# Kernel optimization log

Measured on AMD Instinct MI355X. Metric: run time of the kernel, lower is better.

The kernel has to match this reference:

```python
import jax, jax.numpy as jnp
import numpy as np

N, E, G = 20000, 400000, 200
IN, HID, OUT, H = 8, 64, 32, 4
EPS = 1e-5
NEG_SLOPE = 0.2


def _gatv2(x, src, dst, Wl, bl, Wr, br, att, bias, n, heads, c):
    # lin_l (source messages) and lin_r (target queries)
    xl = (x @ Wl + bl).reshape(n, heads, c)
    xr = (x @ Wr + br).reshape(n, heads, c)
    # per-edge GATv2 score: att . LeakyReLU(x_l[j] + x_r[i])
    e = jax.nn.leaky_relu(xl[src] + xr[dst], NEG_SLOPE)          # [E,H,C]
    score = jnp.einsum('ehc,hc->eh', e, att)                     # [E,H]
    # softmax over incoming edges of each target node
    m = jax.ops.segment_max(score, dst, num_segments=n)
    ex = jnp.exp(score - m[dst])
    den = jax.ops.segment_sum(ex, dst, num_segments=n)
    alpha = ex / den[dst]                                        # [E,H]
    out = jax.ops.segment_sum(alpha[:, :, None] * xl[src], dst, num_segments=n)
    return out.mean(axis=1) + bias                               # concat=False: head mean


def _layernorm(x, g, b):
    mu = x.mean(-1, keepdims=True)
    var = ((x - mu) ** 2).mean(-1, keepdims=True)
    return (x - mu) * jax.lax.rsqrt(var + EPS) * g + b


def setup_inputs() -> dict:
    key = jax.random.key(0)
    ks = jax.random.split(key, 16)
    s = 0.1
    inp = {
        'x': jax.random.normal(ks[0], (N, IN), jnp.float32),
        'edge_index': jax.random.randint(ks[1], (2, E), 0, N, jnp.int64 if jax.config.jax_enable_x64 else jnp.int32),
        'batch': jnp.sort(jax.random.randint(ks[2], (N,), 0, G)),
        'Wl1': jax.random.normal(ks[3], (IN, H * HID), jnp.float32) * s,
        'bl1': jnp.zeros((H * HID,), jnp.float32),
        'Wr1': jax.random.normal(ks[4], (IN, H * HID), jnp.float32) * s,
        'br1': jnp.zeros((H * HID,), jnp.float32),
        'att1': jax.random.normal(ks[5], (H, HID), jnp.float32) * s,
        'b1': jnp.zeros((HID,), jnp.float32),
        'ln1_g': jnp.ones((HID,), jnp.float32),
        'ln1_b': jnp.zeros((HID,), jnp.float32),
        'Wl2': jax.random.normal(ks[6], (HID, H * OUT), jnp.float32) * s,
        'bl2': jnp.zeros((H * OUT,), jnp.float32),
        'Wr2': jax.random.normal(ks[7], (HID, H * OUT), jnp.float32) * s,
        'br2': jnp.zeros((H * OUT,), jnp.float32),
        'att2': jax.random.normal(ks[8], (H, OUT), jnp.float32) * s,
        'b2': jnp.zeros((OUT,), jnp.float32),
        'ln2_g': jnp.ones((OUT,), jnp.float32),
        'ln2_b': jnp.zeros((OUT,), jnp.float32),
    }
    return inp


def reference(x, edge_index, batch, Wl1, bl1, Wr1, br1, att1, b1, ln1_g, ln1_b,
              Wl2, bl2, Wr2, br2, att2, b2, ln2_g, ln2_b):
    n = x.shape[0]
    loop = jnp.arange(n, dtype=edge_index.dtype)  # add_self_loops=True (PyG default)
    src = jnp.concatenate([edge_index[0], loop])
    dst = jnp.concatenate([edge_index[1], loop])

    h = _gatv2(x, src, dst, Wl1, bl1, Wr1, br1, att1, b1, n, H, HID)
    h = jax.nn.relu(_layernorm(h, ln1_g, ln1_b))
    h = _gatv2(h, src, dst, Wl2, bl2, Wr2, br2, att2, b2, n, H, OUT)
    h = jax.nn.relu(_layernorm(h, ln2_g, ln2_b))

    # global mean pool per graph
    cnt = jax.ops.segment_sum(jnp.ones((n,), h.dtype), batch, num_segments=G)
    pooled = jax.ops.segment_sum(h, batch, num_segments=G)
    return pooled / jnp.maximum(cnt, 1.0)[:, None]
```

## Files before the change

kernel.cpp:

```cpp
#include <hip/hip_runtime.h>
#include <math.h>
#include <stdint.h>

#define NEG_SLOPE 0.2f
#define LN_EPS 1e-5f

typedef __attribute__((ext_vector_type(8))) short short8;
typedef __attribute__((ext_vector_type(4))) float f32x4;

__device__ __forceinline__ uint32_t pack_bf2(float a, float b) {
  uint32_t ua = __float_as_uint(a);
  uint32_t ub = __float_as_uint(b);
  ua = (ua + 0x7fffu + ((ua >> 16) & 1u)) >> 16;
  ub = (ub + 0x7fffu + ((ub >> 16) & 1u)) & 0xffff0000u;
  return ua | ub;
}
__device__ __forceinline__ float2 unpack_bf2(uint32_t u) {
  return make_float2(__uint_as_float(u << 16), __uint_as_float(u & 0xffff0000u));
}
__device__ __forceinline__ uint16_t bf16_rne(float f) {
  uint32_t u = __float_as_uint(f);
  return (uint16_t)((u + 0x7fffu + ((u >> 16) & 1u)) >> 16);
}

__global__ void hist_kernel(const int* __restrict__ ei, int E, int N, int* __restrict__ cnt) {
  int e = blockIdx.x * blockDim.x + threadIdx.x;
  if (e >= E + N) return;
  int dst = (e < E) ? ei[E + e] : (e - E);
  atomicAdd(&cnt[dst], 1);
}

__global__ __launch_bounds__(1024) void scan_kernel(const int* __restrict__ cnt,
                                                    int* __restrict__ offs,
                                                    int* __restrict__ cursor, int n) {
  __shared__ int wsum[16];
  int tid = threadIdx.x;
  int lane = tid & 63, w = tid >> 6;
  int PER = (n + 1023) >> 10;
  int base = tid * PER;
  int s = 0;
  for (int j = 0; j < PER; ++j) {
    int idx = base + j;
    s += (idx < n) ? cnt[idx] : 0;
  }
  int inc = s;
#pragma unroll
  for (int d = 1; d < 64; d <<= 1) {
    int t = __shfl_up(inc, d, 64);
    if (lane >= d) inc += t;
  }
  if (lane == 63) wsum[w] = inc;
  __syncthreads();
  int wpre = 0;
  for (int j = 0; j < w; ++j) wpre += wsum[j];
  int run = wpre + inc - s;
  for (int j = 0; j < PER; ++j) {
    int idx = base + j;
    if (idx < n) {
      offs[idx] = run;
      cursor[idx] = run;
      run += cnt[idx];
    }
  }
  if (tid == 1023) offs[n] = run;
}

__global__ void scatter_kernel(const int* __restrict__ ei, int E, int N,
                               int* __restrict__ cursor, int* __restrict__ esrc) {
  int e = blockIdx.x * blockDim.x + threadIdx.x;
  if (e >= E + N) return;
  int src, dst;
  if (e < E) { src = ei[e]; dst = ei[E + e]; }
  else       { src = e - E; dst = src; }
  int pos = atomicAdd(&cursor[dst], 1);
  esrc[pos] = src;
}

__global__ void prep_wt_kernel(const float* __restrict__ Wl, const float* __restrict__ Wr,
                               uint16_t* __restrict__ Wtb) {
  int idx = blockIdx.x * blockDim.x + threadIdx.x;
  if (idx >= 256 * 64) return;
  int c = idx >> 6, k = idx & 63;
  float v = (c < 128) ? Wl[k * 128 + c] : Wr[k * 128 + (c - 128)];
  Wtb[idx] = bf16_rne(v);
}

__global__ __launch_bounds__(256) void gemm1_kernel(
    const float* __restrict__ x,
    const float* __restrict__ Wl, const float* __restrict__ bl,
    const float* __restrict__ Wr, const float* __restrict__ br,
    uint32_t* __restrict__ xl1b, float* __restrict__ xr1, int N) {
  int tid = threadIdx.x;
  int c2 = tid & 127;
  int which = tid >> 7;
  float wl0[8], wl1[8], wr0[8], wr1[8];
#pragma unroll
  for (int k = 0; k < 8; ++k) {
    wl0[k] = Wl[k * 256 + 2 * c2]; wl1[k] = Wl[k * 256 + 2 * c2 + 1];
    wr0[k] = Wr[k * 256 + 2 * c2]; wr1[k] = Wr[k * 256 + 2 * c2 + 1];
  }
  float bl0 = bl[2 * c2], bl1v = bl[2 * c2 + 1];
  float br0 = br[2 * c2], br1v = br[2 * c2 + 1];
  int npair = (N + 1) >> 1;
  for (int pr = blockIdx.x; pr < npair; pr += gridDim.x) {
    int n = pr * 2 + which;
    if (n >= N) continue;
    float4 xa = ((const float4*)x)[n * 2];
    float4 xb = ((const float4*)x)[n * 2 + 1];
    float xs[8] = {xa.x, xa.y, xa.z, xa.w, xb.x, xb.y, xb.z, xb.w};
    float al0 = bl0, al1 = bl1v, ar0 = br0, ar1 = br1v;
#pragma unroll
    for (int k = 0; k < 8; ++k) {
      al0 = fmaf(xs[k], wl0[k], al0); al1 = fmaf(xs[k], wl1[k], al1);
      ar0 = fmaf(xs[k], wr0[k], ar0); ar1 = fmaf(xs[k], wr1[k], ar1);
    }
    xl1b[(size_t)n * 128 + c2] = pack_bf2(al0, al1);
    ((float2*)xr1)[(size_t)n * 128 + c2] = make_float2(ar0, ar1);
  }
}

__global__ __launch_bounds__(256) void gemm2_mfma_kernel(
    const uint16_t* __restrict__ h1b,
    const uint16_t* __restrict__ Wtb,
    const float* __restrict__ bl, const float* __restrict__ br,
    uint32_t* __restrict__ xl2b, float* __restrict__ xr2, int N) {
  int lane = threadIdx.x & 63;
  int w = threadIdx.x >> 6;
  int c0 = w << 6;
  int l15 = lane & 15, l4 = lane >> 4;
  int node = (blockIdx.x << 4) + l15;
  int nodec = node < N ? node : N - 1;
  const short8* hrow = (const short8*)(h1b + (size_t)nodec * 64);
  short8 b0 = hrow[l4];
  short8 b1 = hrow[4 + l4];
  f32x4 acc[4] = {{0.f,0.f,0.f,0.f},{0.f,0.f,0.f,0.f},{0.f,0.f,0.f,0.f},{0.f,0.f,0.f,0.f}};
#pragma unroll
  for (int t = 0; t < 4; ++t) {
    int row = c0 + (t << 4) + l15;
    const short8* wrow = (const short8*)(Wtb + (size_t)row * 64);
    short8 a0 = wrow[l4];
    short8 a1 = wrow[4 + l4];
    acc[t] = __builtin_amdgcn_mfma_f32_16x16x32_bf16(a0, b0, acc[t], 0, 0, 0);
    acc[t] = __builtin_amdgcn_mfma_f32_16x16x32_bf16(a1, b1, acc[t], 0, 0, 0);
  }
  if (node >= N) return;
  if (c0 < 128) {
#pragma unroll
    for (int t = 0; t < 4; ++t) {
      int q0 = c0 + (t << 4) + (l4 << 2);
      float4 bb = *(const float4*)(bl + q0);
      uint2 pk;
      pk.x = pack_bf2(acc[t][0] + bb.x, acc[t][1] + bb.y);
      pk.y = pack_bf2(acc[t][2] + bb.z, acc[t][3] + bb.w);
      *(uint2*)(xl2b + (size_t)node * 64 + (q0 >> 1)) = pk;
    }
  } else {
#pragma unroll
    for (int t = 0; t < 4; ++t) {
      int q0 = (c0 - 128) + (t << 4) + (l4 << 2);
      float4 bb = *(const float4*)(br + q0);
      float4 v = make_float4(acc[t][0] + bb.x, acc[t][1] + bb.y,
                             acc[t][2] + bb.z, acc[t][3] + bb.w);
      *(float4*)(xr2 + (size_t)node * 128 + q0) = v;
    }
  }
}

__global__ __launch_bounds__(256) void attn1_kernel(
    const uint32_t* __restrict__ xl1b, const float* __restrict__ xr1,
    const float* __restrict__ att, const float* __restrict__ b1,
    const float* __restrict__ g, const float* __restrict__ be,
    const int* __restrict__ offs, const int* __restrict__ esrc,
    uint32_t* __restrict__ h1b, int N) {
  int lane = threadIdx.x & 63;
  int i = blockIdx.x * (blockDim.x >> 6) + (threadIdx.x >> 6);
  if (i >= N) return;
  int cq = lane & 15;
  const uint2* xlb = (const uint2*)xl1b;
  float4 attq = ((const float4*)att)[lane];
  float4 attn_ = make_float4(NEG_SLOPE * attq.x, NEG_SLOPE * attq.y,
                             NEG_SLOPE * attq.z, NEG_SLOPE * attq.w);
  float4 xrq = ((const float4*)xr1)[(size_t)i * 64 + lane];
  float dA = 0.f, aA0 = 0.f, aA1 = 0.f, aA2 = 0.f, aA3 = 0.f;
  float dB = 0.f, aB0 = 0.f, aB1 = 0.f, aB2 = 0.f, aB3 = 0.f;
  int beg = offs[i], end = offs[i + 1];
  int p = beg;

#define EDGE1(U, DD, A0, A1, A2, A3)                                           \
  {                                                                            \
    float2 e0 = unpack_bf2(U.x), e1 = unpack_bf2(U.y);                         \
    float t0 = e0.x + xrq.x, t1 = e0.y + xrq.y;                                \
    float t2 = e1.x + xrq.z, t3 = e1.y + xrq.w;                                \
    float sc = t0 * (t0 > 0.f ? attq.x : attn_.x);                             \
    sc = fmaf(t1, (t1 > 0.f ? attq.y : attn_.y), sc);                          \
    sc = fmaf(t2, (t2 > 0.f ? attq.z : attn_.z), sc);                          \
    sc = fmaf(t3, (t3 > 0.f ? attq.w : attn_.w), sc);                          \
    sc += __shfl_xor(sc, 8, 64); sc += __shfl_xor(sc, 4, 64);                  \
    sc += __shfl_xor(sc, 2, 64); sc += __shfl_xor(sc, 1, 64);                  \
    float wgt = __expf(sc);                                                    \
    DD += wgt;                                                                 \
    A0 = fmaf(wgt, e0.x, A0); A1 = fmaf(wgt, e0.y, A1);                        \
    A2 = fmaf(wgt, e1.x, A2); A3 = fmaf(wgt, e1.y, A3);                        \
  }

  for (; p + 3 < end; p += 4) {
    int s0 = esrc[p], s1 = esrc[p + 1], s2 = esrc[p + 2], s3 = esrc[p + 3];
    uint2 u0 = xlb[(size_t)s0 * 64 + lane];
    uint2 u1 = xlb[(size_t)s1 * 64 + lane];
    uint2 u2 = xlb[(size_t)s2 * 64 + lane];
    uint2 u3 = xlb[(size_t)s3 * 64 + lane];
    EDGE1(u0, dA, aA0, aA1, aA2, aA3)
    EDGE1(u1, dB, aB0, aB1, aB2, aB3)
    EDGE1(u2, dA, aA0, aA1, aA2, aA3)
    EDGE1(u3, dB, aB0, aB1, aB2, aB3)
  }
  for (; p < end; ++p) {
    int s0 = esrc[p];
    uint2 u0 = xlb[(size_t)s0 * 64 + lane];
    EDGE1(u0, dA, aA0, aA1, aA2, aA3)
  }
#undef EDGE1

  float inv = 1.0f / (dA + dB);
  float v0 = (aA0 + aB0) * inv;
  float v1 = (aA1 + aB1) * inv;
  float v2 = (aA2 + aB2) * inv;
  float v3 = (aA3 + aB3) * inv;
  v0 += __shfl_xor(v0, 16, 64); v0 += __shfl_xor(v0, 32, 64);
  v1 += __shfl_xor(v1, 16, 64); v1 += __shfl_xor(v1, 32, 64);
  v2 += __shfl_xor(v2, 16, 64); v2 += __shfl_xor(v2, 32, 64);
  v3 += __shfl_xor(v3, 16, 64); v3 += __shfl_xor(v3, 32, 64);
  float4 b1q = ((const float4*)b1)[cq];
  v0 = 0.25f * v0 + b1q.x;
  v1 = 0.25f * v1 + b1q.y;
  v2 = 0.25f * v2 + b1q.z;
  v3 = 0.25f * v3 + b1q.w;
  float s1 = v0 + v1 + v2 + v3;
#pragma unroll
  for (int msk = 8; msk >= 1; msk >>= 1) s1 += __shfl_xor(s1, msk, 64);
  float mu = s1 * (1.0f / 64.0f);
  float d0 = v0 - mu, d1 = v1 - mu, d2 = v2 - mu, d3 = v3 - mu;
  float s2 = d0 * d0 + d1 * d1 + d2 * d2 + d3 * d3;
#pragma unroll
  for (int msk = 8; msk >= 1; msk >>= 1) s2 += __shfl_xor(s2, msk, 64);
  float rstd = rsqrtf(s2 * (1.0f / 64.0f) + LN_EPS);
  float4 gq = ((const float4*)g)[cq];
  float4 beq = ((const float4*)be)[cq];
  float y0 = fmaxf(fmaf(d0 * rstd, gq.x, beq.x), 0.f);
  float y1 = fmaxf(fmaf(d1 * rstd, gq.y, beq.y), 0.f);
  float y2 = fmaxf(fmaf(d2 * rstd, gq.z, beq.z), 0.f);
  float y3 = fmaxf(fmaf(d3 * rstd, gq.w, beq.w), 0.f);
  if (lane < 16) {
    uint2 pk;
    pk.x = pack_bf2(y0, y1);
    pk.y = pack_bf2(y2, y3);
    *(uint2*)(h1b + (size_t)i * 32 + cq * 2) = pk;
  }
}

__global__ __launch_bounds__(256) void attn2_kernel(
    const uint32_t* __restrict__ xl2b, const float* __restrict__ xr2,
    const float* __restrict__ att, const float* __restrict__ b2,
    const float* __restrict__ g, const float* __restrict__ be,
    const int* __restrict__ offs, const int* __restrict__ esrc,
    float* __restrict__ h2, int N) {
  int lane = threadIdx.x & 63;
  int i = blockIdx.x * (blockDim.x >> 6) + (threadIdx.x >> 6);
  if (i >= N) return;
  int cq = lane & 15;
  float2 attq = ((const float2*)att)[lane];
  float2 attn_ = make_float2(NEG_SLOPE * attq.x, NEG_SLOPE * attq.y);
  float2 xrq = ((const float2*)xr2)[(size_t)i * 64 + lane];
  float dA = 0.f, aA0 = 0.f, aA1 = 0.f;
  float dB = 0.f, aB0 = 0.f, aB1 = 0.f;
  int beg = offs[i], end = offs[i + 1];
  int p = beg;

#define EDGE2(U, DD, A0, A1)                                                   \
  {                                                                            \
    float2 e0 = unpack_bf2(U);                                                 \
    float t0 = e0.x + xrq.x, t1 = e0.y + xrq.y;                                \
    float sc = t0 * (t0 > 0.f ? attq.x : attn_.x);                             \
    sc = fmaf(t1, (t1 > 0.f ? attq.y : attn_.y), sc);                          \
    sc += __shfl_xor(sc, 8, 64); sc += __shfl_xor(sc, 4, 64);                  \
    sc += __shfl_xor(sc, 2, 64); sc += __shfl_xor(sc, 1, 64);                  \
    float wgt = __expf(sc);                                                    \
    DD += wgt;                                                                 \
    A0 = fmaf(wgt, e0.x, A0); A1 = fmaf(wgt, e0.y, A1);                        \
  }

  for (; p + 3 < end; p += 4) {
    int s0 = esrc[p], s1 = esrc[p + 1], s2 = esrc[p + 2], s3 = esrc[p + 3];
    uint32_t u0 = xl2b[(size_t)s0 * 64 + lane];
    uint32_t u1 = xl2b[(size_t)s1 * 64 + lane];
    uint32_t u2 = xl2b[(size_t)s2 * 64 + lane];
    uint32_t u3 = xl2b[(size_t)s3 * 64 + lane];
    EDGE2(u0, dA, aA0, aA1)
    EDGE2(u1, dB, aB0, aB1)
    EDGE2(u2, dA, aA0, aA1)
    EDGE2(u3, dB, aB0, aB1)
  }
  for (; p < end; ++p) {
    int s0 = esrc[p];
    uint32_t u0 = xl2b[(size_t)s0 * 64 + lane];
    EDGE2(u0, dA, aA0, aA1)
  }
#undef EDGE2

  float inv = 1.0f / (dA + dB);
  float v0 = (aA0 + aB0) * inv;
  float v1 = (aA1 + aB1) * inv;
  v0 += __shfl_xor(v0, 16, 64); v0 += __shfl_xor(v0, 32, 64);
  v1 += __shfl_xor(v1, 16, 64); v1 += __shfl_xor(v1, 32, 64);
  float2 b2q = ((const float2*)b2)[cq];
  v0 = 0.25f * v0 + b2q.x;
  v1 = 0.25f * v1 + b2q.y;
  float s1 = v0 + v1;
#pragma unroll
  for (int msk = 8; msk >= 1; msk >>= 1) s1 += __shfl_xor(s1, msk, 64);
  float mu = s1 * (1.0f / 32.0f);
  float d0 = v0 - mu, d1 = v1 - mu;
  float s2 = d0 * d0 + d1 * d1;
#pragma unroll
  for (int msk = 8; msk >= 1; msk >>= 1) s2 += __shfl_xor(s2, msk, 64);
  float rstd = rsqrtf(s2 * (1.0f / 32.0f) + LN_EPS);
  float2 gq = ((const float2*)g)[cq];
  float2 beq = ((const float2*)be)[cq];
  float y0 = fmaxf(fmaf(d0 * rstd, gq.x, beq.x), 0.f);
  float y1 = fmaxf(fmaf(d1 * rstd, gq.y, beq.y), 0.f);
  if (lane < 16) ((float2*)h2)[(size_t)i * 16 + cq] = make_float2(y0, y1);
}

__global__ __launch_bounds__(256) void pool_kernel(const float* __restrict__ h2,
                                                   const int* __restrict__ batch,
                                                   float* __restrict__ out, int N) {
  int gidx = blockIdx.x;
  int a = 0, b = N;
  while (a < b) { int m = (a + b) >> 1; if (batch[m] < gidx) a = m + 1; else b = m; }
  int lo = a;
  b = N;
  while (a < b) { int m = (a + b) >> 1; if (batch[m] < gidx + 1) a = m + 1; else b = m; }
  int hi = a;
  int c = threadIdx.x & 31, r = threadIdx.x >> 5;
  float s = 0.f;
  for (int n = lo + r; n < hi; n += 8) s += h2[(size_t)n * 32 + c];
  __shared__ float buf[256];
  buf[threadIdx.x] = s;
  __syncthreads();
  if (threadIdx.x < 128) buf[threadIdx.x] += buf[threadIdx.x + 128];
  __syncthreads();
  if (threadIdx.x < 64) buf[threadIdx.x] += buf[threadIdx.x + 64];
  __syncthreads();
  if (threadIdx.x < 32) {
    float v = buf[threadIdx.x] + buf[threadIdx.x + 32];
    int cnt = hi - lo;
    out[gidx * 32 + threadIdx.x] = v / (float)(cnt > 0 ? cnt : 1);
  }
}

extern "C" void kernel_launch(void* const* d_in, const int* in_sizes, int n_in,
                              void* d_out, int out_size, void* d_ws, size_t ws_size,
                              hipStream_t stream) {
  const float* x    = (const float*)d_in[0];
  const int*   ei   = (const int*)d_in[1];
  const int*   batch= (const int*)d_in[2];
  const float* Wl1  = (const float*)d_in[3];
  const float* bl1  = (const float*)d_in[4];
  const float* Wr1  = (const float*)d_in[5];
  const float* br1  = (const float*)d_in[6];
  const float* att1 = (const float*)d_in[7];
  const float* b1   = (const float*)d_in[8];
  const float* ln1g = (const float*)d_in[9];
  const float* ln1b = (const float*)d_in[10];
  const float* Wl2  = (const float*)d_in[11];
  const float* bl2  = (const float*)d_in[12];
  const float* Wr2  = (const float*)d_in[13];
  const float* br2  = (const float*)d_in[14];
  const float* att2 = (const float*)d_in[15];
  const float* b2   = (const float*)d_in[16];
  const float* ln2g = (const float*)d_in[17];
  const float* ln2b = (const float*)d_in[18];

  int N = in_sizes[0] / 8;
  int E = in_sizes[1] / 2;
  int G = out_size / 32;

  char* ws = (char*)d_ws;
  size_t off = 0;
  auto alloc = [&](size_t bytes) -> void* {
    void* p = (void*)(ws + off);
    off += (bytes + 255) & ~(size_t)255;
    return p;
  };
  int*      cnt    = (int*)alloc((size_t)N * 4);
  int*      offs   = (int*)alloc((size_t)(N + 1) * 4);
  int*      cursor = (int*)alloc((size_t)N * 4);
  int*      esrc   = (int*)alloc((size_t)(E + N) * 4);
  uint32_t* xl1b   = (uint32_t*)alloc((size_t)N * 128 * 4);
  float*    xr1    = (float*)alloc((size_t)N * 256 * 4);
  uint32_t* h1b    = (uint32_t*)alloc((size_t)N * 64 * 2);
  uint16_t* Wtb    = (uint16_t*)alloc((size_t)256 * 64 * 2);
  uint32_t* xl2b   = (uint32_t*)alloc((size_t)N * 64 * 4);
  float*    xr2    = (float*)alloc((size_t)N * 128 * 4);
  float*    h2     = (float*)alloc((size_t)N * 32 * 4);

  hipMemsetAsync(cnt, 0, (size_t)N * 4, stream);

  int tot = E + N;
  hist_kernel<<<(tot + 255) / 256, 256, 0, stream>>>(ei, E, N, cnt);
  scan_kernel<<<1, 1024, 0, stream>>>(cnt, offs, cursor, N);
  scatter_kernel<<<(tot + 255) / 256, 256, 0, stream>>>(ei, E, N, cursor, esrc);
  prep_wt_kernel<<<64, 256, 0, stream>>>(Wl2, Wr2, Wtb);

  gemm1_kernel<<<2048, 256, 0, stream>>>(x, Wl1, bl1, Wr1, br1, xl1b, xr1, N);
  attn1_kernel<<<(N + 3) / 4, 256, 0, stream>>>(xl1b, xr1, att1, b1, ln1g, ln1b,
                                                offs, esrc, h1b, N);
  gemm2_mfma_kernel<<<(N + 15) / 16, 256, 0, stream>>>((const uint16_t*)h1b, Wtb, bl2, br2,
                                                       xl2b, xr2, N);
  attn2_kernel<<<(N + 3) / 4, 256, 0, stream>>>(xl2b, xr2, att2, b2, ln2g, ln2b,
                                                offs, esrc, h2, N);

  pool_kernel<<<G, 256, 0, stream>>>(h2, batch, (float*)d_out, N);
}
```

Baseline: 187.8 us.

## Fuse histogram into gemm1, weight prep into scatter, use DPP row reductions

Merges the destination histogram into the layer-1 linear kernel and the bf16 weight transpose into the CSR scatter kernel, removing two kernel launches. Replaces the xor-shuffle reductions over 16 lanes with DPP row operations, which avoid LDS-based permutes. Switches gather addressing to 32-bit index arithmetic to cut 64-bit multiply work. The fused kernels lengthen serial work inside gemm1 and the scatter, and the 32-bit index math relies on the buffer offsets fitting in 32 bits.

```diff
diff --git a/kernel.cpp b/kernel.cpp
--- a/kernel.cpp
+++ b/kernel.cpp
@@ -23,11 +23,52 @@
   return (uint16_t)((u + 0x7fffu + ((u >> 16) & 1u)) >> 16);
 }
 
-__global__ void hist_kernel(const int* __restrict__ ei, int E, int N, int* __restrict__ cnt) {
-  int e = blockIdx.x * blockDim.x + threadIdx.x;
-  if (e >= E + N) return;
-  int dst = (e < E) ? ei[E + e] : (e - E);
-  atomicAdd(&cnt[dst], 1);
+__device__ __forceinline__ float row16_sum(float x) {
+  x += __int_as_float(__builtin_amdgcn_mov_dpp(__float_as_int(x), 0xB1, 0xF, 0xF, true));
+  x += __int_as_float(__builtin_amdgcn_mov_dpp(__float_as_int(x), 0x4E, 0xF, 0xF, true));
+  x += __int_as_float(__builtin_amdgcn_mov_dpp(__float_as_int(x), 0x124, 0xF, 0xF, true));
+  x += __int_as_float(__builtin_amdgcn_mov_dpp(__float_as_int(x), 0x128, 0xF, 0xF, true));
+  return x;
+}
+
+__global__ __launch_bounds__(256) void gemm1_hist_kernel(
+    const float* __restrict__ x,
+    const float* __restrict__ Wl, const float* __restrict__ bl,
+    const float* __restrict__ Wr, const float* __restrict__ br,
+    uint32_t* __restrict__ xl1b, float* __restrict__ xr1, int N,
+    const int* __restrict__ ei, int E, int* __restrict__ cnt) {
+  int tid = threadIdx.x;
+  int c2 = tid & 127;
+  int which = tid >> 7;
+  float wl0[8], wl1[8], wr0[8], wr1[8];
+#pragma unroll
+  for (int k = 0; k < 8; ++k) {
+    wl0[k] = Wl[k * 256 + 2 * c2]; wl1[k] = Wl[k * 256 + 2 * c2 + 1];
+    wr0[k] = Wr[k * 256 + 2 * c2]; wr1[k] = Wr[k * 256 + 2 * c2 + 1];
+  }
+  float bl0 = bl[2 * c2], bl1v = bl[2 * c2 + 1];
+  float br0 = br[2 * c2], br1v = br[2 * c2 + 1];
+  int npair = (N + 1) >> 1;
+  for (int pr = blockIdx.x; pr < npair; pr += gridDim.x) {
+    int n = pr * 2 + which;
+    if (n >= N) continue;
+    float4 xa = ((const float4*)x)[n * 2];
+    float4 xb = ((const float4*)x)[n * 2 + 1];
+    float xs[8] = {xa.x, xa.y, xa.z, xa.w, xb.x, xb.y, xb.z, xb.w};
+    float al0 = bl0, al1 = bl1v, ar0 = br0, ar1 = br1v;
+#pragma unroll
+    for (int k = 0; k < 8; ++k) {
+      al0 = fmaf(xs[k], wl0[k], al0); al1 = fmaf(xs[k], wl1[k], al1);
+      ar0 = fmaf(xs[k], wr0[k], ar0); ar1 = fmaf(xs[k], wr1[k], ar1);
+    }
+    xl1b[(size_t)n * 128 + c2] = pack_bf2(al0, al1);
+    ((float2*)xr1)[(size_t)n * 128 + c2] = make_float2(ar0, ar1);
+  }
+  int tot = E + N;
+  for (int e = blockIdx.x * blockDim.x + tid; e < tot; e += gridDim.x * blockDim.x) {
+    int dst = (e < E) ? ei[E + e] : (e - E);
+    atomicAdd(&cnt[dst], 1);
+  }
 }
 
 __global__ __launch_bounds__(1024) void scan_kernel(const int* __restrict__ cnt,
@@ -66,7 +107,15 @@
 }
 
 __global__ void scatter_kernel(const int* __restrict__ ei, int E, int N,
-                               int* __restrict__ cursor, int* __restrict__ esrc) {
+                               int* __restrict__ cursor, int* __restrict__ esrc,
+                               const float* __restrict__ Wl2, const float* __restrict__ Wr2,
+                               uint16_t* __restrict__ Wtb) {
+  if (blockIdx.x < 64) {
+    int idx = blockIdx.x * 256 + threadIdx.x;
+    int c = idx >> 6, k = idx & 63;
+    float v = (c < 128) ? Wl2[k * 128 + c] : Wr2[k * 128 + (c - 128)];
+    Wtb[idx] = bf16_rne(v);
+  }
   int e = blockIdx.x * blockDim.x + threadIdx.x;
   if (e >= E + N) return;
   int src, dst;
@@ -74,49 +123,6 @@
   else       { src = e - E; dst = src; }
   int pos = atomicAdd(&cursor[dst], 1);
   esrc[pos] = src;
-}
-
-__global__ void prep_wt_kernel(const float* __restrict__ Wl, const float* __restrict__ Wr,
-                               uint16_t* __restrict__ Wtb) {
-  int idx = blockIdx.x * blockDim.x + threadIdx.x;
-  if (idx >= 256 * 64) return;
-  int c = idx >> 6, k = idx & 63;
-  float v = (c < 128) ? Wl[k * 128 + c] : Wr[k * 128 + (c - 128)];
-  Wtb[idx] = bf16_rne(v);
-}
-
-__global__ __launch_bounds__(256) void gemm1_kernel(
-    const float* __restrict__ x,
-    const float* __restrict__ Wl, const float* __restrict__ bl,
-    const float* __restrict__ Wr, const float* __restrict__ br,
-    uint32_t* __restrict__ xl1b, float* __restrict__ xr1, int N) {
-  int tid = threadIdx.x;
-  int c2 = tid & 127;
-  int which = tid >> 7;
-  float wl0[8], wl1[8], wr0[8], wr1[8];
-#pragma unroll
-  for (int k = 0; k < 8; ++k) {
-    wl0[k] = Wl[k * 256 + 2 * c2]; wl1[k] = Wl[k * 256 + 2 * c2 + 1];
-    wr0[k] = Wr[k * 256 + 2 * c2]; wr1[k] = Wr[k * 256 + 2 * c2 + 1];
-  }
-  float bl0 = bl[2 * c2], bl1v = bl[2 * c2 + 1];
-  float br0 = br[2 * c2], br1v = br[2 * c2 + 1];
-  int npair = (N + 1) >> 1;
-  for (int pr = blockIdx.x; pr < npair; pr += gridDim.x) {
-    int n = pr * 2 + which;
-    if (n >= N) continue;
-    float4 xa = ((const float4*)x)[n * 2];
-    float4 xb = ((const float4*)x)[n * 2 + 1];
-    float xs[8] = {xa.x, xa.y, xa.z, xa.w, xb.x, xb.y, xb.z, xb.w};
-    float al0 = bl0, al1 = bl1v, ar0 = br0, ar1 = br1v;
-#pragma unroll
-    for (int k = 0; k < 8; ++k) {
-      al0 = fmaf(xs[k], wl0[k], al0); al1 = fmaf(xs[k], wl1[k], al1);
-      ar0 = fmaf(xs[k], wr0[k], ar0); ar1 = fmaf(xs[k], wr1[k], ar1);
-    }
-    xl1b[(size_t)n * 128 + c2] = pack_bf2(al0, al1);
-    ((float2*)xr1)[(size_t)n * 128 + c2] = make_float2(ar0, ar1);
-  }
 }
 
 __global__ __launch_bounds__(256) void gemm2_mfma_kernel(
@@ -195,8 +201,7 @@
     sc = fmaf(t1, (t1 > 0.f ? attq.y : attn_.y), sc);                          \
     sc = fmaf(t2, (t2 > 0.f ? attq.z : attn_.z), sc);                          \
     sc = fmaf(t3, (t3 > 0.f ? attq.w : attn_.w), sc);                          \
-    sc += __shfl_xor(sc, 8, 64); sc += __shfl_xor(sc, 4, 64);                  \
-    sc += __shfl_xor(sc, 2, 64); sc += __shfl_xor(sc, 1, 64);                  \
+    sc = row16_sum(sc);                                                        \
     float wgt = __expf(sc);                                                    \
     DD += wgt;                                                                 \
     A0 = fmaf(wgt, e0.x, A0); A1 = fmaf(wgt, e0.y, A1);                        \
@@ -205,10 +210,10 @@
 
   for (; p + 3 < end; p += 4) {
     int s0 = esrc[p], s1 = esrc[p + 1], s2 = esrc[p + 2], s3 = esrc[p + 3];
-    uint2 u0 = xlb[(size_t)s0 * 64 + lane];
-    uint2 u1 = xlb[(size_t)s1 * 64 + lane];
-    uint2 u2 = xlb[(size_t)s2 * 64 + lane];
-    uint2 u3 = xlb[(size_t)s3 * 64 + lane];
+    uint2 u0 = xlb[(uint32_t)s0 * 64u + lane];
+    uint2 u1 = xlb[(uint32_t)s1 * 64u + lane];
+    uint2 u2 = xlb[(uint32_t)s2 * 64u + lane];
+    uint2 u3 = xlb[(uint32_t)s3 * 64u + lane];
     EDGE1(u0, dA, aA0, aA1, aA2, aA3)
     EDGE1(u1, dB, aB0, aB1, aB2, aB3)
     EDGE1(u2, dA, aA0, aA1, aA2, aA3)
@@ -216,7 +221,7 @@
   }
   for (; p < end; ++p) {
     int s0 = esrc[p];
-    uint2 u0 = xlb[(size_t)s0 * 64 + lane];
+    uint2 u0 = xlb[(uint32_t)s0 * 64u + lane];
     EDGE1(u0, dA, aA0, aA1, aA2, aA3)
   }
 #undef EDGE1
@@ -235,14 +240,10 @@
   v1 = 0.25f * v1 + b1q.y;
   v2 = 0.25f * v2 + b1q.z;
   v3 = 0.25f * v3 + b1q.w;
-  float s1 = v0 + v1 + v2 + v3;
-#pragma unroll
-  for (int msk = 8; msk >= 1; msk >>= 1) s1 += __shfl_xor(s1, msk, 64);
+  float s1 = row16_sum(v0 + v1 + v2 + v3);
   float mu = s1 * (1.0f / 64.0f);
   float d0 = v0 - mu, d1 = v1 - mu, d2 = v2 - mu, d3 = v3 - mu;
-  float s2 = d0 * d0 + d1 * d1 + d2 * d2 + d3 * d3;
-#pragma unroll
-  for (int msk = 8; msk >= 1; msk >>= 1) s2 += __shfl_xor(s2, msk, 64);
+  float s2 = row16_sum(d0 * d0 + d1 * d1 + d2 * d2 + d3 * d3);
   float rstd = rsqrtf(s2 * (1.0f / 64.0f) + LN_EPS);
   float4 gq = ((const float4*)g)[cq];
   float4 beq = ((const float4*)be)[cq];
@@ -282,8 +283,7 @@
     float t0 = e0.x + xrq.x, t1 = e0.y + xrq.y;                                \
     float sc = t0 * (t0 > 0.f ? attq.x : attn_.x);                             \
     sc = fmaf(t1, (t1 > 0.f ? attq.y : attn_.y), sc);                          \
-    sc += __shfl_xor(sc, 8, 64); sc += __shfl_xor(sc, 4, 64);                  \
-    sc += __shfl_xor(sc, 2, 64); sc += __shfl_xor(sc, 1, 64);                  \
+    sc = row16_sum(sc);                                                        \
     float wgt = __expf(sc);                                                    \
     DD += wgt;                                                                 \
     A0 = fmaf(wgt, e0.x, A0); A1 = fmaf(wgt, e0.y, A1);                        \
@@ -291,10 +291,10 @@
 
   for (; p + 3 < end; p += 4) {
     int s0 = esrc[p], s1 = esrc[p + 1], s2 = esrc[p + 2], s3 = esrc[p + 3];
-    uint32_t u0 = xl2b[(size_t)s0 * 64 + lane];
-    uint32_t u1 = xl2b[(size_t)s1 * 64 + lane];
-    uint32_t u2 = xl2b[(size_t)s2 * 64 + lane];
-    uint32_t u3 = xl2b[(size_t)s3 * 64 + lane];
+    uint32_t u0 = xl2b[(uint32_t)s0 * 64u + lane];
+    uint32_t u1 = xl2b[(uint32_t)s1 * 64u + lane];
+    uint32_t u2 = xl2b[(uint32_t)s2 * 64u + lane];
+    uint32_t u3 = xl2b[(uint32_t)s3 * 64u + lane];
     EDGE2(u0, dA, aA0, aA1)
     EDGE2(u1, dB, aB0, aB1)
     EDGE2(u2, dA, aA0, aA1)
@@ -302,7 +302,7 @@
   }
   for (; p < end; ++p) {
     int s0 = esrc[p];
-    uint32_t u0 = xl2b[(size_t)s0 * 64 + lane];
+    uint32_t u0 = xl2b[(uint32_t)s0 * 64u + lane];
     EDGE2(u0, dA, aA0, aA1)
   }
 #undef EDGE2
@@ -315,14 +315,10 @@
   float2 b2q = ((const float2*)b2)[cq];
   v0 = 0.25f * v0 + b2q.x;
   v1 = 0.25f * v1 + b2q.y;
-  float s1 = v0 + v1;
-#pragma unroll
-  for (int msk = 8; msk >= 1; msk >>= 1) s1 += __shfl_xor(s1, msk, 64);
+  float s1 = row16_sum(v0 + v1);
   float mu = s1 * (1.0f / 32.0f);
   float d0 = v0 - mu, d1 = v1 - mu;
-  float s2 = d0 * d0 + d1 * d1;
-#pragma unroll
-  for (int msk = 8; msk >= 1; msk >>= 1) s2 += __shfl_xor(s2, msk, 64);
+  float s2 = row16_sum(d0 * d0 + d1 * d1);
   float rstd = rsqrtf(s2 * (1.0f / 32.0f) + LN_EPS);
   float2 gq = ((const float2*)g)[cq];
   float2 beq = ((const float2*)be)[cq];
@@ -407,12 +403,12 @@
   hipMemsetAsync(cnt, 0, (size_t)N * 4, stream);
 
   int tot = E + N;
-  hist_kernel<<<(tot + 255) / 256, 256, 0, stream>>>(ei, E, N, cnt);
+  gemm1_hist_kernel<<<2048, 256, 0, stream>>>(x, Wl1, bl1, Wr1, br1, xl1b, xr1, N,
+                                              ei, E, cnt);
   scan_kernel<<<1, 1024, 0, stream>>>(cnt, offs, cursor, N);
-  scatter_kernel<<<(tot + 255) / 256, 256, 0, stream>>>(ei, E, N, cursor, esrc);
-  prep_wt_kernel<<<64, 256, 0, stream>>>(Wl2, Wr2, Wtb);
-
-  gemm1_kernel<<<2048, 256, 0, stream>>>(x, Wl1, bl1, Wr1, br1, xl1b, xr1, N);
+  scatter_kernel<<<(tot + 255) / 256, 256, 0, stream>>>(ei, E, N, cursor, esrc,
+                                                        Wl2, Wr2, Wtb);
+
   attn1_kernel<<<(N + 3) / 4, 256, 0, stream>>>(xl1b, xr1, att1, b1, ln1g, ln1b,
                                                 offs, esrc, h1b, N);
   gemm2_mfma_kernel<<<(N + 15) / 16, 256, 0, stream>>>((const uint16_t*)h1b, Wtb, bl2, br2,
```

After: 173.6 us. 1.08x faster.
